# Kernel tuning notes

Measured on AMD Instinct MI355X. Metric: run time of the kernel, lower is better.

Reference implementation:

```python
import jax, jax.numpy as jnp
import numpy as np

N_NODES = 50000
N_EDGES = 800000
N_GRAPHS = 512
D = 128
NUM_GIN_LAYERS = 4
BN_EPS = 1e-5


def setup_inputs() -> dict:
    key = jax.random.key(0)
    ks = jax.random.split(key, 10)
    h = jax.random.normal(ks[0], (N_NODES, D), dtype=jnp.float32)
    src = jax.random.randint(ks[1], (N_EDGES,), 0, N_NODES, dtype=jnp.int32)
    dst = jax.random.randint(ks[2], (N_EDGES,), 0, N_NODES, dtype=jnp.int32)
    graph_id = jnp.sort(jax.random.randint(ks[3], (N_NODES,), 0, N_GRAPHS, dtype=jnp.int32))
    scale = 1.0 / np.sqrt(D)
    W1s = jax.random.normal(ks[4], (NUM_GIN_LAYERS, D, D), dtype=jnp.float32) * scale
    W2s = jax.random.normal(ks[5], (NUM_GIN_LAYERS, D, D), dtype=jnp.float32) * scale
    bn1_g = jnp.ones((NUM_GIN_LAYERS, D), jnp.float32)
    bn1_b = jnp.zeros((NUM_GIN_LAYERS, D), jnp.float32)
    bn2_g = jnp.ones((NUM_GIN_LAYERS, D), jnp.float32)
    bn2_b = jnp.zeros((NUM_GIN_LAYERS, D), jnp.float32)
    pred_W = jax.random.normal(ks[6], (NUM_GIN_LAYERS + 1, D, D), dtype=jnp.float32) * scale
    pred_b = jnp.zeros((NUM_GIN_LAYERS + 1, D), jnp.float32)
    return {"h": h, "src": src, "dst": dst, "graph_id": graph_id,
            "W1s": W1s, "W2s": W2s, "bn1_g": bn1_g, "bn1_b": bn1_b,
            "bn2_g": bn2_g, "bn2_b": bn2_b, "pred_W": pred_W, "pred_b": pred_b}


def _batch_norm(x, gamma, beta):
    # training-mode BN over the node axis
    mean = jnp.mean(x, axis=0)
    var = jnp.var(x, axis=0)
    return (x - mean) * jax.lax.rsqrt(var + BN_EPS) * gamma + beta


def reference(h, src, dst, graph_id, W1s, W2s, bn1_g, bn1_b, bn2_g, bn2_b, pred_W, pred_b):
    n = h.shape[0]
    hidden_rep = [h]
    for i in range(NUM_GIN_LAYERS):
        # GINConv, eps=0: (1+eps)*h + sum over in-neighbors (scatter-sum over edges)
        agg = jax.ops.segment_sum(h[src], dst, num_segments=n)
        z = h + agg
        # two-layer MLP: Linear(no bias) -> BN -> ReLU -> Linear(no bias)
        z = jax.nn.relu(_batch_norm(z @ W1s[i], bn1_g[i], bn1_b[i]))
        z = z @ W2s[i]
        # outer BN + ReLU
        h = jax.nn.relu(_batch_norm(z, bn2_g[i], bn2_b[i]))
        hidden_rep.append(h)
    # graph readout: per-graph max pool over each layer's representation,
    # then per-layer linear prediction summed (dropout is identity in eval)
    score = jnp.zeros((N_GRAPHS, pred_W.shape[-1]), h.dtype)
    for i, hr in enumerate(hidden_rep):
        pooled = jax.ops.segment_max(hr, graph_id, num_segments=N_GRAPHS,
                                     indices_are_sorted=True)
        score = score + pooled @ pred_W[i] + pred_b[i]
    return score
```

## Files before the change

### kernel.cpp

```cpp
#include <hip/hip_runtime.h>

#define N_NODES 50000
#define N_EDGES 800000
#define N_GRAPHS 512
#define DIM 128
#define NLAYERS 4
#define BN_EPS 1e-5f
#define NTILE (N_NODES / 16)
#define POIS ((int)0xAAAAAAAA)
#define NREP 8

#define NBUCK 80
#define CAPB 12288
#define EPB 1600
#define NBIN 500

typedef unsigned short u16;
typedef float f32x2 __attribute__((ext_vector_type(2)));
typedef float f32x4 __attribute__((ext_vector_type(4)));
typedef short bf16x8 __attribute__((ext_vector_type(8)));

__device__ __forceinline__ short f2bs(float f) {
    union { float f; unsigned u; } v; v.f = f;
    unsigned r = v.u + 0x7FFFu + ((v.u >> 16) & 1u);
    return (short)(r >> 16);
}
__device__ __forceinline__ float bu2f(unsigned u) {
    union { unsigned u; float f; } v; v.u = u << 16;
    return v.f;
}
__device__ __forceinline__ unsigned packbf(float x, float y) {
    return ((unsigned)(u16)f2bs(y) << 16) | (unsigned)(u16)f2bs(x);
}

__device__ __forceinline__ void foldbn(const float* __restrict__ st,
                                       const float* __restrict__ gamma,
                                       const float* __restrict__ beta,
                                       float* absm, int tid) {
    if (tid < 128) {
        float s = 0.f, sq = 0.f;
#pragma unroll
        for (int j = 0; j < NREP; j++) {
            s += st[j * 256 + tid];
            sq += st[j * 256 + 128 + tid];
        }
        float mean = s * (1.f / N_NODES);
        float var = sq * (1.f / N_NODES) - mean * mean;
        float a = gamma[tid] * rsqrtf(var + BN_EPS);
        absm[tid] = a;
        absm[DIM + tid] = beta[tid] - mean * a;
    }
}

__global__ __launch_bounds__(256) void k_prepbin(const float* __restrict__ h,
                                                 const float* __restrict__ W1s,
                                                 const float* __restrict__ W2s,
                                                 const int* __restrict__ gid,
                                                 const int* __restrict__ src,
                                                 const int* __restrict__ dst,
                                                 unsigned* __restrict__ hb,
                                                 short* __restrict__ wt,
                                                 int* __restrict__ gs, int* __restrict__ ge,
                                                 unsigned* __restrict__ eb,
                                                 int* __restrict__ gcur) {
    __shared__ int hist[NBUCK], base[NBUCK], lcur[NBUCK];
    int bid = blockIdx.x, tid = threadIdx.x;
    if (bid >= 6250) {
        int bbid = bid - 6250;
        if (tid < NBUCK) hist[tid] = 0;
        __syncthreads();
        int e0 = bbid * EPB;
        unsigned rec[7]; int rb[7];
#pragma unroll
        for (int k = 0; k < 7; k++) {
            int idx = tid + k * 256;
            rb[k] = -1;
            if (idx < EPB) {
                int s = src[e0 + idx], d = dst[e0 + idx];
                rec[k] = ((unsigned)d << 16) | (unsigned)s;
                int x = d / 6250;
                int sub = (d - x * 6250) / 625;
                rb[k] = x + 8 * sub;
                atomicAdd(&hist[rb[k]], 1);
            }
        }
        __syncthreads();
        if (tid < NBUCK) {
            int old = atomicAdd(&gcur[tid], hist[tid]);
            base[tid] = old - POIS;
            lcur[tid] = 0;
        }
        __syncthreads();
#pragma unroll
        for (int k = 0; k < 7; k++) {
            if (rb[k] >= 0) {
                int p = atomicAdd(&lcur[rb[k]], 1);
                eb[rb[k] * CAPB + base[rb[k]] + p] = rec[k];
            }
        }
        return;
    }
    int gtid = bid * 256 + tid;
    {
        f32x4 v = *(const f32x4*)(h + gtid * 4);
        uint2 pp;
        pp.x = packbf(v.x, v.y);
        pp.y = packbf(v.z, v.w);
        *(uint2*)(hb + gtid * 2) = pp;
    }
    if (gtid < 8 * 16384) {
        int m = gtid >> 14, r = gtid & 16383, n = r >> 7, k = r & 127;
        const float* W = (m < 4) ? (W1s + m * 16384) : (W2s + (m - 4) * 16384);
        wt[gtid] = f2bs(W[k * DIM + n]);
    }
    if (gtid < N_NODES) {
        int g = gid[gtid];
        if (gtid == 0 || gid[gtid - 1] != g) gs[g] = gtid;
        if (gtid == N_NODES - 1 || gid[gtid + 1] != g) ge[g] = gtid + 1;
    }
}

__global__ __launch_bounds__(256) void k_fillpool0(const unsigned* __restrict__ eb,
                                                   const int* __restrict__ gcur,
                                                   int* __restrict__ begA,
                                                   int* __restrict__ endA,
                                                   u16* __restrict__ eix,
                                                   const float* __restrict__ h,
                                                   const int* __restrict__ gs,
                                                   const int* __restrict__ ge,
                                                   float* __restrict__ pool4) {
    __shared__ int hist[625], begL[625], sm[256];
    __shared__ f32x2 psm[256];
    int bid = blockIdx.x, tid = threadIdx.x;
    if (bid < NBUCK) {
        int x = bid & 7, sub = bid >> 3;
        int n0 = x * 6250 + sub * 625;
        int mybase = 0, mycnt = 0;
        for (int r = 0; r < NBUCK; r++) {
            int c = gcur[r] - POIS;
            int rx = r & 7, rs = r >> 3;
            if (rx < x || (rx == x && rs < sub)) mybase += c;
            if (r == bid) mycnt = c;
        }
        for (int i = tid; i < 625; i += 256) hist[i] = 0;
        __syncthreads();
        const unsigned* my = eb + bid * CAPB;
        for (int i = tid; i < mycnt; i += 256) {
            int dl = (int)(my[i] >> 16) - n0;
            atomicAdd(&hist[dl], 1);
        }
        __syncthreads();
        int carry = 0;
        for (int c = 0; c < 3; c++) {
            int idx = c * 256 + tid;
            int v = (idx < 625) ? hist[idx] : 0;
            int xv = v;
            sm[tid] = xv; __syncthreads();
#pragma unroll
            for (int d = 1; d < 256; d <<= 1) {
                int y = (tid >= d) ? sm[tid - d] : 0;
                __syncthreads();
                sm[tid] = xv = xv + y;
                __syncthreads();
            }
            if (idx < 625) begL[idx] = mybase + carry + xv - v;
            int ct = sm[255];
            __syncthreads();
            carry += ct;
        }
        __syncthreads();
        for (int i = tid; i < 625; i += 256) {
            int b = begL[i];
            begA[n0 + i] = b;
            endA[n0 + i] = b + hist[i];
        }
        __syncthreads();
        for (int i = tid; i < mycnt; i += 256) {
            unsigned rc = my[i];
            int dl = (int)(rc >> 16) - n0;
            int p = atomicAdd(&begL[dl], 1);
            eix[p] = (u16)(rc & 0xFFFFu);
        }
        return;
    }
    int pb = bid - NBUCK;
    int g = pb >> 2, sub = pb & 3;
    int c2 = (tid & 63) * 2, ro = tid >> 6;
    int beg = gs[g], end = ge[g];
    f32x2 mx = (f32x2){-3.402823e38f, -3.402823e38f};
    if (beg >= 0 && end <= N_NODES) {
        for (int r = beg + sub * 4 + ro; r < end; r += 16) {
            f32x2 v = *(const f32x2*)(h + r * DIM + c2);
            mx.x = fmaxf(mx.x, v.x);
            mx.y = fmaxf(mx.y, v.y);
        }
    }
    psm[tid] = mx;
    __syncthreads();
    if (ro == 0) {
        f32x2 mA0 = psm[tid], mA1 = psm[tid + 64];
        f32x2 mB0 = psm[tid + 128], mB1 = psm[tid + 192];
        f32x2 a, b;
        a.x = fmaxf(mA0.x, mA1.x); a.y = fmaxf(mA0.y, mA1.y);
        b.x = fmaxf(mB0.x, mB1.x); b.y = fmaxf(mB0.y, mB1.y);
        *(f32x2*)(pool4 + (pb * 2) * DIM + c2) = a;
        *(f32x2*)(pool4 + (pb * 2 + 1) * DIM + c2) = b;
    }
}

__global__ __launch_bounds__(128) void k_gather0(const unsigned* __restrict__ hp,
                                                 const int* __restrict__ begA,
                                                 const int* __restrict__ endA,
                                                 const u16* __restrict__ eix,
                                                 unsigned* __restrict__ Za) {
    int node = blockIdx.x * 2 + (threadIdx.x >> 6);
    int lane = threadIdx.x & 63;
    float ax = 0.f, ay = 0.f;
#define TX(w, rx, ry)                                         \
    {                                                         \
        rx += bu2f((w) & 0xffffu); ry += bu2f((w) >> 16);     \
    }
    TX(hp[node * 64 + lane], ax, ay);
    int beg = begA[node];
    int end = endA[node];
    int e = beg;
    if ((e & 1) && e < end) {
        unsigned ww = hp[eix[e] * 64 + lane];
        TX(ww, ax, ay);
        e++;
    }
    const unsigned* ep = (const unsigned*)eix;
    for (; e + 8 <= end; e += 8) {
        int k = e >> 1;
        unsigned p0 = ep[k], p1 = ep[k + 1], p2 = ep[k + 2], p3 = ep[k + 3];
        unsigned w0 = hp[(p0 & 0xffffu) * 64 + lane], w1 = hp[(p0 >> 16) * 64 + lane];
        unsigned w2 = hp[(p1 & 0xffffu) * 64 + lane], w3 = hp[(p1 >> 16) * 64 + lane];
        unsigned w4 = hp[(p2 & 0xffffu) * 64 + lane], w5 = hp[(p2 >> 16) * 64 + lane];
        unsigned w6 = hp[(p3 & 0xffffu) * 64 + lane], w7 = hp[(p3 >> 16) * 64 + lane];
        TX(w0, ax, ay); TX(w1, ax, ay); TX(w2, ax, ay); TX(w3, ax, ay);
        TX(w4, ax, ay); TX(w5, ax, ay); TX(w6, ax, ay); TX(w7, ax, ay);
    }
    for (; e + 2 <= end; e += 2) {
        unsigned pp = ep[e >> 1];
        unsigned w0 = hp[(pp & 0xffffu) * 64 + lane], w1 = hp[(pp >> 16) * 64 + lane];
        TX(w0, ax, ay); TX(w1, ax, ay);
    }
    if (e < end) {
        unsigned ww = hp[eix[e] * 64 + lane];
        TX(ww, ax, ay);
    }
#undef TX
    Za[node * 64 + lane] = packbf(ax, ay);
}

__global__ __launch_bounds__(128) void k_poolgather(const unsigned* __restrict__ Zr,
                                                    const float* __restrict__ stats,
                                                    const float* __restrict__ gamma,
                                                    const float* __restrict__ beta,
                                                    const int* __restrict__ gs,
                                                    const int* __restrict__ ge,
                                                    float* __restrict__ pool4,
                                                    const int* __restrict__ begA,
                                                    const int* __restrict__ endA,
                                                    const u16* __restrict__ eix,
                                                    unsigned* __restrict__ Za) {
    __shared__ float absm[256];
    __shared__ f32x2 psm[128];
    int bid = blockIdx.x, tid = threadIdx.x;
    foldbn(stats, gamma, beta, absm, tid);
    __syncthreads();
    if (bid < 4096) {
        int g = bid >> 3, sub = bid & 7;
        int ci = tid & 63, ro = tid >> 6;
        int beg = gs[g], end = ge[g];
        f32x2 a = *(const f32x2*)(absm + ci * 2);
        f32x2 b = *(const f32x2*)(absm + DIM + ci * 2);
        f32x2 mx = (f32x2){-3.402823e38f, -3.402823e38f};
        if (beg >= 0 && end <= N_NODES) {
            for (int r = beg + sub * 2 + ro; r < end; r += 16) {
                unsigned w = Zr[r * 64 + ci];
                float vx = fmaxf(a.x * bu2f(w & 0xffffu) + b.x, 0.f);
                float vy = fmaxf(a.y * bu2f(w >> 16) + b.y, 0.f);
                mx.x = fmaxf(mx.x, vx);
                mx.y = fmaxf(mx.y, vy);
            }
        }
        psm[tid] = mx;
        __syncthreads();
        if (ro == 0) {
            f32x2 m0 = psm[tid], m1 = psm[tid + 64];
            m0.x = fmaxf(m0.x, m1.x);
            m0.y = fmaxf(m0.y, m1.y);
            *(f32x2*)(pool4 + bid * DIM + ci * 2) = m0;
        }
        return;
    }
    int node = (bid - 4096) * 2 + (tid >> 6);
    int lane = tid & 63;
    float a0 = absm[2 * lane], a1 = absm[2 * lane + 1];
    float b0 = absm[DIM + 2 * lane], b1 = absm[DIM + 2 * lane + 1];
#define TX(w, rx, ry)                                         \
    {                                                         \
        float _x = bu2f((w) & 0xffffu), _y = bu2f((w) >> 16); \
        _x = fmaxf(a0 * _x + b0, 0.f);                        \
        _y = fmaxf(a1 * _y + b1, 0.f);                        \
        rx += _x; ry += _y;                                   \
    }
    float ax = 0.f, ay = 0.f;
    TX(Zr[node * 64 + lane], ax, ay);
    int beg = begA[node];
    int end = endA[node];
    int e = beg;
    if ((e & 1) && e < end) {
        unsigned ww = Zr[eix[e] * 64 + lane];
        TX(ww, ax, ay);
        e++;
    }
    const unsigned* ep = (const unsigned*)eix;
    for (; e + 8 <= end; e += 8) {
        int k = e >> 1;
        unsigned p0 = ep[k], p1 = ep[k + 1], p2 = ep[k + 2], p3 = ep[k + 3];
        unsigned w0 = Zr[(p0 & 0xffffu) * 64 + lane], w1 = Zr[(p0 >> 16) * 64 + lane];
        unsigned w2 = Zr[(p1 & 0xffffu) * 64 + lane], w3 = Zr[(p1 >> 16) * 64 + lane];
        unsigned w4 = Zr[(p2 & 0xffffu) * 64 + lane], w5 = Zr[(p2 >> 16) * 64 + lane];
        unsigned w6 = Zr[(p3 & 0xffffu) * 64 + lane], w7 = Zr[(p3 >> 16) * 64 + lane];
        TX(w0, ax, ay); TX(w1, ax, ay); TX(w2, ax, ay); TX(w3, ax, ay);
        TX(w4, ax, ay); TX(w5, ax, ay); TX(w6, ax, ay); TX(w7, ax, ay);
    }
    for (; e + 2 <= end; e += 2) {
        unsigned pp = ep[e >> 1];
        unsigned w0 = Zr[(pp & 0xffffu) * 64 + lane], w1 = Zr[(pp >> 16) * 64 + lane];
        TX(w0, ax, ay); TX(w1, ax, ay);
    }
    if (e < end) {
        unsigned ww = Zr[eix[e] * 64 + lane];
        TX(ww, ax, ay);
    }
#undef TX
    Za[node * 64 + lane] = packbf(ax, ay);
}

template <bool XF>
__global__ __launch_bounds__(256, 2) void k_gemm(const unsigned* __restrict__ X,
                                                 const short* __restrict__ wt,
                                                 const float* __restrict__ statsPrev,
                                                 const float* __restrict__ gamma,
                                                 const float* __restrict__ beta,
                                                 unsigned* __restrict__ OUT,
                                                 float* __restrict__ statsDst) {
    __shared__ float tbuf[4][16][68];
    __shared__ float absm[256];
    __shared__ float smst[256];
    const int tid = threadIdx.x, bid = blockIdx.x;
    const int lane = tid & 63, wid = tid >> 6;
    const int ln15 = lane & 15, q = lane >> 4;
    float (*buf)[68] = tbuf[wid];

    bf16x8 bfr[8][4];
#pragma unroll
    for (int tl = 0; tl < 8; tl++)
#pragma unroll
        for (int s = 0; s < 4; s++)
            bfr[tl][s] = *(const bf16x8*)(wt + (tl * 16 + ln15) * DIM + s * 32 + q * 8);

    if (XF) foldbn(statsPrev, gamma, beta, absm, tid);
    smst[tid] = 0.f;
    __syncthreads();

    float sac[8], qac[8];
#pragma unroll
    for (int t = 0; t < 8; t++) { sac[t] = 0.f; qac[t] = 0.f; }

    f32x4 aA[4], aB[4], bA[4], bB[4];
    if (XF) {
#pragma unroll
        for (int s = 0; s < 4; s++) {
            int k0 = s * 32 + q * 8;
            aA[s] = *(const f32x4*)(absm + k0);
            aB[s] = *(const f32x4*)(absm + k0 + 4);
            bA[s] = *(const f32x4*)(absm + DIM + k0);
            bB[s] = *(const f32x4*)(absm + DIM + k0 + 4);
        }
    }

    int tile = bid + 512 * wid;
    uint4 wv[4];
    if (tile < NTILE) {
        const unsigned* xr = X + (tile * 16 + ln15) * 64;
#pragma unroll
        for (int s = 0; s < 4; s++) wv[s] = *(const uint4*)(xr + s * 16 + q * 4);
    }
    while (tile < NTILE) {
        int nt = tile + 2048;
        uint4 nwv[4];
        if (nt < NTILE) {
            const unsigned* xr2 = X + (nt * 16 + ln15) * 64;
#pragma unroll
            for (int s = 0; s < 4; s++) nwv[s] = *(const uint4*)(xr2 + s * 16 + q * 4);
        }
        bf16x8 afr[4];
        if constexpr (!XF) {
#pragma unroll
            for (int s = 0; s < 4; s++) afr[s] = *(bf16x8*)&wv[s];
        } else {
#pragma unroll
            for (int s = 0; s < 4; s++) {
                uint4 w4v = wv[s];
                float v0 = fmaxf(aA[s].x * bu2f(w4v.x & 0xffffu) + bA[s].x, 0.f);
                float v1 = fmaxf(aA[s].y * bu2f(w4v.x >> 16) + bA[s].y, 0.f);
                float v2 = fmaxf(aA[s].z * bu2f(w4v.y & 0xffffu) + bA[s].z, 0.f);
                float v3 = fmaxf(aA[s].w * bu2f(w4v.y >> 16) + bA[s].w, 0.f);
                float v4 = fmaxf(aB[s].x * bu2f(w4v.z & 0xffffu) + bB[s].x, 0.f);
                float v5 = fmaxf(aB[s].y * bu2f(w4v.z >> 16) + bB[s].y, 0.f);
                float v6 = fmaxf(aB[s].z * bu2f(w4v.w & 0xffffu) + bB[s].z, 0.f);
                float v7 = fmaxf(aB[s].w * bu2f(w4v.w >> 16) + bB[s].w, 0.f);
                bf16x8 a;
                a[0] = f2bs(v0); a[1] = f2bs(v1); a[2] = f2bs(v2); a[3] = f2bs(v3);
                a[4] = f2bs(v4); a[5] = f2bs(v5); a[6] = f2bs(v6); a[7] = f2bs(v7);
                afr[s] = a;
            }
        }
        f32x4 acc[8];
#pragma unroll
        for (int t = 0; t < 8; t++) acc[t] = (f32x4){0.f, 0.f, 0.f, 0.f};
#pragma unroll
        for (int s = 0; s < 4; s++) {
#pragma unroll
            for (int t = 0; t < 8; t++)
                acc[t] = __builtin_amdgcn_mfma_f32_16x16x32_bf16(afr[s], bfr[t][s], acc[t], 0, 0, 0);
        }
#pragma unroll
        for (int t = 0; t < 8; t++) {
            float s_l = 0.f, q_l = 0.f;
#pragma unroll
            for (int r = 0; r < 4; r++) {
                float v = acc[t][r];
                s_l += v;
                q_l += v * v;
            }
            s_l += __shfl_xor(s_l, 16); s_l += __shfl_xor(s_l, 32);
            q_l += __shfl_xor(q_l, 16); q_l += __shfl_xor(q_l, 32);
            sac[t] += s_l;
            qac[t] += q_l;
        }
#pragma unroll
        for (int ch = 0; ch < 2; ch++) {
#pragma unroll
            for (int t2 = 0; t2 < 4; t2++) {
                int t = ch * 4 + t2;
#pragma unroll
                for (int r = 0; r < 4; r++)
                    buf[q * 4 + r][t2 * 16 + ln15] = acc[t][r];
            }
#pragma unroll
            for (int rr = 0; rr < 4; rr++) {
                int lr = rr * 4 + q;
                f32x4 v = *(const f32x4*)&buf[lr][ln15 * 4];
                uint2 pp;
                pp.x = packbf(v.x, v.y);
                pp.y = packbf(v.z, v.w);
                *(uint2*)(OUT + (tile * 16 + lr) * 64 + ch * 32 + ln15 * 2) = pp;
            }
        }
        tile = nt;
#pragma unroll
        for (int s = 0; s < 4; s++) wv[s] = nwv[s];
    }
    if (lane < 16) {
#pragma unroll
        for (int t = 0; t < 8; t++) {
            atomicAdd(&smst[t * 16 + ln15], sac[t]);
            atomicAdd(&smst[128 + t * 16 + ln15], qac[t]);
        }
    }
    __syncthreads();
    atomicAdd(statsDst + (bid & (NREP - 1)) * 256 + tid, smst[tid]);
}

__global__ __launch_bounds__(256) void k_pool(const unsigned* __restrict__ Zr,
                                              const float* __restrict__ stats,
                                              const float* __restrict__ gamma,
                                              const float* __restrict__ beta,
                                              const int* __restrict__ gs,
                                              const int* __restrict__ ge,
                                              float* __restrict__ pool4) {
    __shared__ float absm[256];
    __shared__ f32x2 psm[256];
    int bid = blockIdx.x, tid = threadIdx.x;
    int g = bid >> 2, sub = bid & 3;
    foldbn(stats, gamma, beta, absm, tid);
    __syncthreads();
    int ci = tid & 63, ro = tid >> 6;
    int beg = gs[g], end = ge[g];
    f32x2 a = *(const f32x2*)(absm + ci * 2);
    f32x2 b = *(const f32x2*)(absm + DIM + ci * 2);
    f32x2 mx = (f32x2){-3.402823e38f, -3.402823e38f};
    if (beg >= 0 && end <= N_NODES) {
        for (int r = beg + sub * 4 + ro; r < end; r += 16) {
            unsigned w = Zr[r * 64 + ci];
            float vx = fmaxf(a.x * bu2f(w & 0xffffu) + b.x, 0.f);
            float vy = fmaxf(a.y * bu2f(w >> 16) + b.y, 0.f);
            mx.x = fmaxf(mx.x, vx);
            mx.y = fmaxf(mx.y, vy);
        }
    }
    psm[tid] = mx;
    __syncthreads();
    if (ro == 0) {
        f32x2 mA0 = psm[tid], mA1 = psm[tid + 64];
        f32x2 mB0 = psm[tid + 128], mB1 = psm[tid + 192];
        f32x2 aa, bb;
        aa.x = fmaxf(mA0.x, mA1.x); aa.y = fmaxf(mA0.y, mA1.y);
        bb.x = fmaxf(mB0.x, mB1.x); bb.y = fmaxf(mB0.y, mB1.y);
        *(f32x2*)(pool4 + (bid * 2) * DIM + ci * 2) = aa;
        *(f32x2*)(pool4 + (bid * 2 + 1) * DIM + ci * 2) = bb;
    }
}

__global__ __launch_bounds__(640) void k_readout(const float* __restrict__ pool4,
                                                 const float* __restrict__ predW,
                                                 const float* __restrict__ predb,
                                                 float* __restrict__ out) {
    __shared__ float pl[5][DIM];
    __shared__ float ps[5][DIM];
    int g = blockIdx.x, t = threadIdx.x;
    int l = t >> 7, c = t & 127;
    {
        const float* p = pool4 + l * (N_GRAPHS * 8 * DIM) + g * 8 * DIM + c;
        float m = p[0];
#pragma unroll
        for (int j = 1; j < 8; j++) m = fmaxf(m, p[j * DIM]);
        pl[l][c] = m;
    }
    __syncthreads();
    float acc = 0.f;
    const float* W = predW + l * DIM * DIM;
    const float* prow = pl[l];
#pragma unroll 8
    for (int k = 0; k < DIM; k++) acc += prow[k] * W[k * DIM + c];
    ps[l][c] = acc;
    __syncthreads();
    if (t < DIM) {
        float s = 0.f;
#pragma unroll
        for (int ll = 0; ll < 5; ll++) s += ps[ll][c] + predb[ll * DIM + c];
        out[g * DIM + c] = s;
    }
}

extern "C" void kernel_launch(void* const* d_in, const int* in_sizes, int n_in,
                              void* d_out, int out_size, void* d_ws, size_t ws_size,
                              hipStream_t stream) {
    const float* h_in = (const float*)d_in[0];
    const int* src = (const int*)d_in[1];
    const int* dst = (const int*)d_in[2];
    const int* gid = (const int*)d_in[3];
    const float* W1s = (const float*)d_in[4];
    const float* W2s = (const float*)d_in[5];
    const float* bn1g = (const float*)d_in[6];
    const float* bn1b = (const float*)d_in[7];
    const float* bn2g = (const float*)d_in[8];
    const float* bn2b = (const float*)d_in[9];
    const float* predW = (const float*)d_in[10];
    const float* predb = (const float*)d_in[11];

    char* ws = (char*)d_ws;
    unsigned* hb = (unsigned*)(ws);
    unsigned* Za = (unsigned*)(ws + 12800000);
    unsigned* Yb = (unsigned*)(ws + 25600000);
    unsigned* Zr = (unsigned*)(ws + 38400000);
    short* wt = (short*)(ws + 51200000);
    float* pool4 = (float*)(ws + 51527680);
    int* begA = (int*)(ws + 62013440);
    int* endA = (int*)(ws + 62213440);
    u16* eix = (u16*)(ws + 62413440);
    int* gs = (int*)(ws + 64013440);
    int* ge = (int*)(ws + 64015488);
    float* stats = (float*)(ws + 64017536);
    unsigned* eb = (unsigned*)(ws + 25600000);
    int* gcur = (int*)(ws + 25600000 + 8388608);
    float* out = (float*)d_out;

    const int PSTRIDE = N_GRAPHS * 8 * DIM;

    k_prepbin<<<6750, 256, 0, stream>>>(h_in, W1s, W2s, gid, src, dst, hb, wt, gs, ge, eb, gcur);
    k_fillpool0<<<NBUCK + 2048, 256, 0, stream>>>(eb, gcur, begA, endA, eix, h_in, gs, ge, pool4);

    k_gather0<<<25000, 128, 0, stream>>>(hb, begA, endA, eix, Za);
    k_gemm<false><<<512, 256, 0, stream>>>(Za, wt + 0 * 16384, nullptr, nullptr, nullptr,
                                           Yb, stats + 0 * (NREP * 256));
    k_gemm<true><<<512, 256, 0, stream>>>(Yb, wt + 4 * 16384, stats + 0 * (NREP * 256),
                                          bn1g, bn1b, Zr, stats + 1 * (NREP * 256));
    for (int l = 1; l < NLAYERS; l++) {
        k_poolgather<<<29096, 128, 0, stream>>>(Zr, stats + ((l - 1) * 2 + 1) * (NREP * 256),
                                                bn2g + (l - 1) * DIM, bn2b + (l - 1) * DIM,
                                                gs, ge, pool4 + l * PSTRIDE,
                                                begA, endA, eix, Za);
        k_gemm<false><<<512, 256, 0, stream>>>(Za, wt + l * 16384, nullptr, nullptr, nullptr,
                                               Yb, stats + (l * 2) * (NREP * 256));
        k_gemm<true><<<512, 256, 0, stream>>>(Yb, wt + (4 + l) * 16384,
                                              stats + (l * 2) * (NREP * 256), bn1g + l * DIM,
                                              bn1b + l * DIM, Zr,
                                              stats + (l * 2 + 1) * (NREP * 256));
    }
    k_pool<<<2048, 256, 0, stream>>>(Zr, stats + 7 * (NREP * 256), bn2g + 3 * DIM,
                                     bn2b + 3 * DIM, gs, ge, pool4 + 4 * PSTRIDE);
    k_readout<<<512, 640, 0, stream>>>(pool4, predW, predb, out);
}
```

Measured before the change: 470.7 us.

## Stage GEMM weights in LDS and assign one tile per wave

The bf16 weight matrix now lives in shared memory instead of a large per-thread register array, and the fused GEMM kernel's launch bounds go from 2 to 3 blocks per SM. The persistent grid-stride loop with register prefetch of the next tile is replaced by a 782-block grid in which each wave handles exactly one 16-row tile. The number of BN-stat replicas is raised from 8 to 32 to spread the global atomics. The aim is higher occupancy and less register pressure. The cost is repeated LDS reads of the B fragments, the loss of software prefetch, and a per-block weight load repeated across many more blocks.

```diff
diff --git a/kernel.cpp b/kernel.cpp
--- a/kernel.cpp
+++ b/kernel.cpp
@@ -8,7 +8,7 @@
 #define BN_EPS 1e-5f
 #define NTILE (N_NODES / 16)
 #define POIS ((int)0xAAAAAAAA)
-#define NREP 8
+#define NREP 32
 
 #define NBUCK 80
 #define CAPB 12288
@@ -341,13 +341,14 @@
 }
 
 template <bool XF>
-__global__ __launch_bounds__(256, 2) void k_gemm(const unsigned* __restrict__ X,
+__global__ __launch_bounds__(256, 3) void k_gemm(const unsigned* __restrict__ X,
                                                  const short* __restrict__ wt,
                                                  const float* __restrict__ statsPrev,
                                                  const float* __restrict__ gamma,
                                                  const float* __restrict__ beta,
                                                  unsigned* __restrict__ OUT,
                                                  float* __restrict__ statsDst) {
+    __shared__ short wls[128][136];
     __shared__ float tbuf[4][16][68];
     __shared__ float absm[256];
     __shared__ float smst[256];
@@ -356,13 +357,13 @@
     const int ln15 = lane & 15, q = lane >> 4;
     float (*buf)[68] = tbuf[wid];
 
-    bf16x8 bfr[8][4];
-#pragma unroll
-    for (int tl = 0; tl < 8; tl++)
-#pragma unroll
-        for (int s = 0; s < 4; s++)
-            bfr[tl][s] = *(const bf16x8*)(wt + (tl * 16 + ln15) * DIM + s * 32 + q * 8);
-
+    {
+        int r = tid >> 1, hh = tid & 1;
+        const uint4* s4 = (const uint4*)(wt + r * 128 + hh * 64);
+        uint4* d4 = (uint4*)&wls[r][hh * 64];
+#pragma unroll
+        for (int i = 0; i < 8; i++) d4[i] = s4[i];
+    }
     if (XF) foldbn(statsPrev, gamma, beta, absm, tid);
     smst[tid] = 0.f;
     __syncthreads();
@@ -371,41 +372,29 @@
 #pragma unroll
     for (int t = 0; t < 8; t++) { sac[t] = 0.f; qac[t] = 0.f; }
 
-    f32x4 aA[4], aB[4], bA[4], bB[4];
-    if (XF) {
-#pragma unroll
-        for (int s = 0; s < 4; s++) {
-            int k0 = s * 32 + q * 8;
-            aA[s] = *(const f32x4*)(absm + k0);
-            aB[s] = *(const f32x4*)(absm + k0 + 4);
-            bA[s] = *(const f32x4*)(absm + DIM + k0);
-            bB[s] = *(const f32x4*)(absm + DIM + k0 + 4);
-        }
-    }
-
-    int tile = bid + 512 * wid;
-    uint4 wv[4];
+    int tile = bid * 4 + wid;
     if (tile < NTILE) {
+        f32x4 aA[4], aB[4], bA[4], bB[4];
+        if (XF) {
+#pragma unroll
+            for (int s = 0; s < 4; s++) {
+                int k0 = s * 32 + q * 8;
+                aA[s] = *(const f32x4*)(absm + k0);
+                aB[s] = *(const f32x4*)(absm + k0 + 4);
+                bA[s] = *(const f32x4*)(absm + DIM + k0);
+                bB[s] = *(const f32x4*)(absm + DIM + k0 + 4);
+            }
+        }
         const unsigned* xr = X + (tile * 16 + ln15) * 64;
-#pragma unroll
-        for (int s = 0; s < 4; s++) wv[s] = *(const uint4*)(xr + s * 16 + q * 4);
-    }
-    while (tile < NTILE) {
-        int nt = tile + 2048;
-        uint4 nwv[4];
-        if (nt < NTILE) {
-            const unsigned* xr2 = X + (nt * 16 + ln15) * 64;
-#pragma unroll
-            for (int s = 0; s < 4; s++) nwv[s] = *(const uint4*)(xr2 + s * 16 + q * 4);
-        }
         bf16x8 afr[4];
         if constexpr (!XF) {
 #pragma unroll
-            for (int s = 0; s < 4; s++) afr[s] = *(bf16x8*)&wv[s];
+            for (int s = 0; s < 4; s++)
+                afr[s] = *(const bf16x8*)(xr + s * 16 + q * 4);
         } else {
 #pragma unroll
             for (int s = 0; s < 4; s++) {
-                uint4 w4v = wv[s];
+                uint4 w4v = *(const uint4*)(xr + s * 16 + q * 4);
                 float v0 = fmaxf(aA[s].x * bu2f(w4v.x & 0xffffu) + bA[s].x, 0.f);
                 float v1 = fmaxf(aA[s].y * bu2f(w4v.x >> 16) + bA[s].y, 0.f);
                 float v2 = fmaxf(aA[s].z * bu2f(w4v.y & 0xffffu) + bA[s].z, 0.f);
@@ -426,8 +415,10 @@
 #pragma unroll
         for (int s = 0; s < 4; s++) {
 #pragma unroll
-            for (int t = 0; t < 8; t++)
-                acc[t] = __builtin_amdgcn_mfma_f32_16x16x32_bf16(afr[s], bfr[t][s], acc[t], 0, 0, 0);
+            for (int t = 0; t < 8; t++) {
+                bf16x8 bfr = *(const bf16x8*)&wls[t * 16 + ln15][s * 32 + q * 8];
+                acc[t] = __builtin_amdgcn_mfma_f32_16x16x32_bf16(afr[s], bfr, acc[t], 0, 0, 0);
+            }
         }
 #pragma unroll
         for (int t = 0; t < 8; t++) {
@@ -440,8 +431,8 @@
             }
             s_l += __shfl_xor(s_l, 16); s_l += __shfl_xor(s_l, 32);
             q_l += __shfl_xor(q_l, 16); q_l += __shfl_xor(q_l, 32);
-            sac[t] += s_l;
-            qac[t] += q_l;
+            sac[t] = s_l;
+            qac[t] = q_l;
         }
 #pragma unroll
         for (int ch = 0; ch < 2; ch++) {
@@ -462,9 +453,6 @@
                 *(uint2*)(OUT + (tile * 16 + lr) * 64 + ch * 32 + ln15 * 2) = pp;
             }
         }
-        tile = nt;
-#pragma unroll
-        for (int s = 0; s < 4; s++) wv[s] = nwv[s];
     }
     if (lane < 16) {
 #pragma unroll
@@ -587,18 +575,18 @@
     k_fillpool0<<<NBUCK + 2048, 256, 0, stream>>>(eb, gcur, begA, endA, eix, h_in, gs, ge, pool4);
 
     k_gather0<<<25000, 128, 0, stream>>>(hb, begA, endA, eix, Za);
-    k_gemm<false><<<512, 256, 0, stream>>>(Za, wt + 0 * 16384, nullptr, nullptr, nullptr,
+    k_gemm<false><<<782, 256, 0, stream>>>(Za, wt + 0 * 16384, nullptr, nullptr, nullptr,
                                            Yb, stats + 0 * (NREP * 256));
-    k_gemm<true><<<512, 256, 0, stream>>>(Yb, wt + 4 * 16384, stats + 0 * (NREP * 256),
+    k_gemm<true><<<782, 256, 0, stream>>>(Yb, wt + 4 * 16384, stats + 0 * (NREP * 256),
                                           bn1g, bn1b, Zr, stats + 1 * (NREP * 256));
     for (int l = 1; l < NLAYERS; l++) {
         k_poolgather<<<29096, 128, 0, stream>>>(Zr, stats + ((l - 1) * 2 + 1) * (NREP * 256),
                                                 bn2g + (l - 1) * DIM, bn2b + (l - 1) * DIM,
                                                 gs, ge, pool4 + l * PSTRIDE,
                                                 begA, endA, eix, Za);
-        k_gemm<false><<<512, 256, 0, stream>>>(Za, wt + l * 16384, nullptr, nullptr, nullptr,
+        k_gemm<false><<<782, 256, 0, stream>>>(Za, wt + l * 16384, nullptr, nullptr, nullptr,
                                                Yb, stats + (l * 2) * (NREP * 256));
-        k_gemm<true><<<512, 256, 0, stream>>>(Yb, wt + (4 + l) * 16384,
+        k_gemm<true><<<782, 256, 0, stream>>>(Yb, wt + (4 + l) * 16384,
                                               stats + (l * 2) * (NREP * 256), bn1g + l * DIM,
                                               bn1b + l * DIM, Zr,
                                               stats + (l * 2 + 1) * (NREP * 256));
```

Result: slower. 490.1 us (+4.1%).
